# Kernel tuning notes

Measured on AMD Instinct MI355X. Metric: run time of the kernel, lower is better.

The kernel has to match this reference:

```python
import jax, jax.numpy as jnp
import numpy as np

B, N, C, H, K, R = 128, 512, 7, 64, 16, 2
EPS = 1e-5


def setup_inputs() -> dict:
    key = jax.random.key(0)
    ks = jax.random.split(key, 8)
    def w(k, shape, scale):
        return jax.random.normal(k, shape, jnp.float32) * scale
    return {
        'x':    jax.random.normal(ks[0], (B, C, N), jnp.float32),
        # track_mlp: Conv1d(C->H, bias=False) + BN + ReLU, Conv1d(H->H) + BN + ReLU
        'w_t1': w(ks[1], (H, C), 0.3),
        'g_t1': jnp.ones((H,), jnp.float32), 'b_t1': jnp.zeros((H,), jnp.float32),
        'w_t2': w(ks[2], (H, H), 0.15),
        'g_t2': jnp.ones((H,), jnp.float32), 'b_t2': jnp.zeros((H,), jnp.float32),
        # per-round neighbor MLP: Conv1d(2H->H, bias=False) + BN + ReLU (stacked over rounds)
        'w_nb': w(ks[3], (R, H, 2 * H), 0.1),
        'g_nb': jnp.ones((R, H), jnp.float32), 'b_nb': jnp.zeros((R, H), jnp.float32),
        # scorer: Conv1d(H->H, bias=False) + BN + ReLU, Conv1d(H->1, bias=True)
        'w_s1': w(ks[4], (H, H), 0.15),
        'g_s1': jnp.ones((H,), jnp.float32), 'b_s1': jnp.zeros((H,), jnp.float32),
        'w_s2': w(ks[5], (1, H), 0.15), 'b_s2': jnp.zeros((1,), jnp.float32),
    }


def _conv1x1(w, h):
    # Conv1d with kernel_size=1, no bias: (O,C) x (B,C,N) -> (B,O,N)
    return jnp.einsum('oc,bcn->bon', w, h)


def _bn(h, g, b):
    # eval-mode BatchNorm1d with running_mean=0, running_var=1
    s = g / jnp.sqrt(1.0 + EPS)
    return h * s[None, :, None] + b[None, :, None]


def _knn_idx(h, k):
    # h: (B,H,N); squared euclidean distances in feature space, k nearest (incl. self)
    sq = jnp.sum(h * h, axis=1)                       # (B,N)
    inner = jnp.einsum('bhn,bhm->bnm', h, h)          # (B,N,N)
    d = sq[:, :, None] + sq[:, None, :] - 2.0 * inner  # (B,N,N)
    _, idx = jax.lax.top_k(-d, k)                     # (B,N,K)
    return jax.lax.stop_gradient(idx)


def _edgeconv_round(h, w, g, b, k):
    idx = _knn_idx(h, k)                              # (B,N,K)
    # gather neighbor features: (B,H,1,N) indexed along last axis -> (B,H,N,K)
    nbr = jnp.take_along_axis(h[:, :, None, :], idx[:, None, :, :], axis=3)
    hc = h[:, :, :, None]                             # (B,H,N,1)
    edge = jnp.concatenate([jnp.broadcast_to(hc, nbr.shape), nbr - hc], axis=1)  # (B,2H,N,K)
    bsz, twoh, n, kk = edge.shape
    m = _conv1x1(w, edge.reshape(bsz, twoh, n * kk))  # (B,H,N*K)
    m = jax.nn.relu(_bn(m, g, b)).reshape(bsz, -1, n, kk)
    return jnp.max(m, axis=3)                          # (B,H,N) max aggregation


def reference(x, w_t1, g_t1, b_t1, w_t2, g_t2, b_t2, w_nb, g_nb, b_nb,
              w_s1, g_s1, b_s1, w_s2, b_s2):
    # shared per-track MLP
    h = jax.nn.relu(_bn(_conv1x1(w_t1, x), g_t1, b_t1))
    h = jax.nn.relu(_bn(_conv1x1(w_t2, h), g_t2, b_t2))
    # kNN message-passing rounds (EdgeConv with max aggregation)
    for r in range(w_nb.shape[0]):
        h = _edgeconv_round(h, w_nb[r], g_nb[r], b_nb[r], K)
    # scorer head -> per-track logits (B,1,N)
    h = jax.nn.relu(_bn(_conv1x1(w_s1, h), g_s1, b_s1))
    logits = _conv1x1(w_s2, h) + b_s2[None, :, None]
    return logits
```

## Files before the change

kernel.cpp:

```cpp
#include <hip/hip_runtime.h>
#include <math.h>

#define Bn 128
#define Nn 512
#define Cc 7
#define Hh 64
#define Kk 16
#define Rr 2
#define EPSf 1e-5f

typedef __attribute__((ext_vector_type(8))) short bf16x8;
typedef __attribute__((ext_vector_type(4))) float f32x4;

#define PLN ((size_t)4194304)

__device__ __forceinline__ void split3(float a, short &hs, short &ms, short &ls) {
    unsigned u  = __float_as_uint(a);
    unsigned hu = u & 0xFFFF0000u;
    float r1 = a - __uint_as_float(hu);
    unsigned mu = __float_as_uint(r1) & 0xFFFF0000u;
    float r2 = r1 - __uint_as_float(mu);
    unsigned lu = __float_as_uint(r2) & 0xFFFF0000u;
    hs = (short)(hu >> 16); ms = (short)(mu >> 16); ls = (short)(lu >> 16);
}

#define MFMA6(acc, AH, AM, AL, BH, BM, BL) \
    acc = __builtin_amdgcn_mfma_f32_16x16x32_bf16(AL, BH, acc, 0, 0, 0); \
    acc = __builtin_amdgcn_mfma_f32_16x16x32_bf16(AM, BM, acc, 0, 0, 0); \
    acc = __builtin_amdgcn_mfma_f32_16x16x32_bf16(AH, BL, acc, 0, 0, 0); \
    acc = __builtin_amdgcn_mfma_f32_16x16x32_bf16(AM, BH, acc, 0, 0, 0); \
    acc = __builtin_amdgcn_mfma_f32_16x16x32_bf16(AH, BM, acc, 0, 0, 0); \
    acc = __builtin_amdgcn_mfma_f32_16x16x32_bf16(AH, BH, acc, 0, 0, 0);

__global__ void k_prep(const float* __restrict__ w_nb, const float* __restrict__ w_t2,
                       const float* __restrict__ w_s1, short* __restrict__ wS)
{
    int i = blockIdx.x * 256 + threadIdx.x;
    short h_, m_, l_;
    if (i < 8192) {
        int r = i >> 12, oc = i & 4095;
        int o = oc >> 6, c = oc & 63;
        const float* wr = w_nb + (size_t)r * Hh * 2 * Hh + (size_t)o * 2 * Hh;
        float wc = wr[c], wd = wr[Hh + c];
        short* base = wS + (size_t)r * 6 * 4096;
        split3(wd, h_, m_, l_);
        base[0 * 4096 + oc] = h_; base[1 * 4096 + oc] = m_; base[2 * 4096 + oc] = l_;
        split3(wc - wd, h_, m_, l_);
        base[3 * 4096 + oc] = h_; base[4 * 4096 + oc] = m_; base[5 * 4096 + oc] = l_;
    } else {
        int which = (i - 8192) >> 12;
        int oc = i & 4095;
        const float* src = which ? w_s1 : w_t2;
        short* base = wS + (size_t)(12 + which * 3) * 4096;
        split3(src[oc], h_, m_, l_);
        base[0 * 4096 + oc] = h_; base[1 * 4096 + oc] = m_; base[2 * 4096 + oc] = l_;
    }
}

__global__ __launch_bounds__(256) void k_t12(
    const float* __restrict__ x,
    const float* __restrict__ w1, const float* __restrict__ g1, const float* __restrict__ b1,
    const short* __restrict__ wS2, const float* __restrict__ g2, const float* __restrict__ b2,
    short* __restrict__ hS, float* __restrict__ sq)
{
    __shared__ short wLDS[3][64 * 80];
    __shared__ short h1S[3][16 * 80];
    __shared__ float sqP[16][4];

    int t  = threadIdx.x;
    int p0 = blockIdx.x * 16;
    int b  = p0 >> 9, n0 = p0 & 511;

#pragma unroll
    for (int it = 0; it < 6; ++it) {
        int f = it * 256 + t;
        int plane = f >> 9, i8 = f & 511;
        int o = i8 >> 3, c8 = i8 & 7;
        uint4 v = ((const uint4*)(wS2 + (size_t)plane * 4096))[i8];
        *(uint4*)&wLDS[plane][o * 80 + c8 * 8] = v;
    }

    {
        int pt = t & 15, ow = t >> 4;
        const float inv = rsqrtf(1.0f + EPSf);
        float xv[Cc];
#pragma unroll
        for (int c = 0; c < Cc; ++c)
            xv[c] = x[(b * Cc + c) * Nn + n0 + pt];
#pragma unroll
        for (int j = 0; j < 4; ++j) {
            int o = ow + 16 * j;
            float acc = 0.0f;
#pragma unroll
            for (int c = 0; c < Cc; ++c)
                acc = fmaf(w1[o * Cc + c], xv[c], acc);
            acc = fmaf(acc, g1[o] * inv, b1[o]);
            acc = fmaxf(acc, 0.0f);
            short hs_, ms_, ls_;
            split3(acc, hs_, ms_, ls_);
            h1S[0][pt * 80 + o] = hs_;
            h1S[1][pt * 80 + o] = ms_;
            h1S[2][pt * 80 + o] = ls_;
        }
    }
    __syncthreads();

    int wv = t >> 6, lane = t & 63, col = lane & 15, quad = lane >> 4;
    const float inv = rsqrtf(1.0f + EPSf);

    f32x4 acc = (f32x4){0.f, 0.f, 0.f, 0.f};
#pragma unroll
    for (int ks = 0; ks < 2; ++ks) {
        int aoff = ks * 32 + quad * 8;
        bf16x8 AH = *(bf16x8*)&h1S[0][col * 80 + aoff];
        bf16x8 AM = *(bf16x8*)&h1S[1][col * 80 + aoff];
        bf16x8 AL = *(bf16x8*)&h1S[2][col * 80 + aoff];
        int boff = (wv * 16 + col) * 80 + aoff;
        bf16x8 BH = *(bf16x8*)&wLDS[0][boff];
        bf16x8 BM = *(bf16x8*)&wLDS[1][boff];
        bf16x8 BL = *(bf16x8*)&wLDS[2][boff];
        MFMA6(acc, AH, AM, AL, BH, BM, BL)
    }

    int o = wv * 16 + col;
    float sc = g2[o] * inv, bo = b2[o];
    float s4[4];
#pragma unroll
    for (int r = 0; r < 4; ++r) {
        int pt = quad * 4 + r;
        float a2 = fmaf(acc[r], sc, bo);
        a2 = fmaxf(a2, 0.0f);
        short hs_, ms_, ls_;
        split3(a2, hs_, ms_, ls_);
        size_t rowp = (size_t)(p0 + pt) * Hh + o;
        hS[0 * PLN + rowp] = hs_;
        hS[1 * PLN + rowp] = ms_;
        hS[2 * PLN + rowp] = ls_;
        s4[r] = a2 * a2;
    }
#pragma unroll
    for (int sh = 1; sh < 16; sh <<= 1) {
#pragma unroll
        for (int r = 0; r < 4; ++r) s4[r] += __shfl_xor(s4[r], sh, 64);
    }
    if (col == 0) {
#pragma unroll
        for (int r = 0; r < 4; ++r) sqP[quad * 4 + r][wv] = s4[r];
    }
    __syncthreads();
    if (t < 16) sq[p0 + t] = sqP[t][0] + sqP[t][1] + sqP[t][2] + sqP[t][3];
}

__global__ __launch_bounds__(256, 4) void k_knn(
    const short* __restrict__ hS, const float* __restrict__ sq, int* __restrict__ idxout)
{
    int xcd = blockIdx.x & 7;
    int s_  = blockIdx.x >> 3;
    int b   = xcd + ((s_ >> 5) << 3);
    int n0  = (s_ & 31) << 4;
    int t   = threadIdx.x;

    __shared__ unsigned int keysLDS[16 * 512];
    __shared__ float sqS[512];

    if (t < 128) ((float4*)sqS)[t] = ((const float4*)(sq + (size_t)b * Nn))[t];
    __syncthreads();

    int wv = t >> 6, lane = t & 63, col = lane & 15, quad = lane >> 4;
    const size_t rowbase = (size_t)b * Nn * Hh;

    bf16x8 AH[2], AM[2], AL[2];
    {
        const short* crow = hS + rowbase + (size_t)(n0 + col) * Hh;
#pragma unroll
        for (int ks = 0; ks < 2; ++ks) {
            int aoff = ks * 32 + quad * 8;
            AH[ks] = *(const bf16x8*)(crow + 0 * PLN + aoff);
            AM[ks] = *(const bf16x8*)(crow + 1 * PLN + aoff);
            AL[ks] = *(const bf16x8*)(crow + 2 * PLN + aoff);
        }
    }
    float sqcr[4];
#pragma unroll
    for (int r_ = 0; r_ < 4; ++r_) sqcr[r_] = sqS[n0 + quad * 4 + r_];

    for (int i = 0; i < 8; ++i) {
        int nt = wv * 8 + i;
        const short* prow = hS + rowbase + (size_t)(nt * 16 + col) * Hh;
        f32x4 acc = (f32x4){0.f, 0.f, 0.f, 0.f};
#pragma unroll
        for (int ks = 0; ks < 2; ++ks) {
            int aoff = ks * 32 + quad * 8;
            bf16x8 BH = *(const bf16x8*)(prow + 0 * PLN + aoff);
            bf16x8 BM = *(const bf16x8*)(prow + 1 * PLN + aoff);
            bf16x8 BL = *(const bf16x8*)(prow + 2 * PLN + aoff);
            MFMA6(acc, AH[ks], AM[ks], AL[ks], BH, BM, BL)
        }
        float sqp = sqS[nt * 16 + col];
#pragma unroll
        for (int r_ = 0; r_ < 4; ++r_) {
            int ctr = quad * 4 + r_;
            float d = sqcr[r_] + sqp - 2.0f * acc[r_];
            unsigned int u = __float_as_uint(d);
            u = ((int)u < 0) ? ~u : (u | 0x80000000u);
            keysLDS[ctr * 512 + nt * 16 + col] = u;
        }
    }
    __syncthreads();

    for (int pass = 0; pass < 2; ++pass) {
        unsigned int kk[2][8];
        int rr[2][8];
#pragma unroll
        for (int s = 0; s < 2; ++s) {
            int jj = wv * 4 + pass * 2 + s;
            const uint4* kp = (const uint4*)&keysLDS[jj * 512 + (lane << 3)];
            uint4 A = kp[0], Bq = kp[1];
            kk[s][0] = A.x;  kk[s][1] = A.y;  kk[s][2] = A.z;  kk[s][3] = A.w;
            kk[s][4] = Bq.x; kk[s][5] = Bq.y; kk[s][6] = Bq.z; kk[s][7] = Bq.w;
#pragma unroll
            for (int q = 0; q < 8; ++q) rr[s][q] = q;
        }

#define CE(s, i, j_) { \
    bool sw = (kk[s][i] > kk[s][j_]) || (kk[s][i] == kk[s][j_] && rr[s][i] > rr[s][j_]); \
    unsigned int tk = sw ? kk[s][i] : kk[s][j_]; kk[s][i] = sw ? kk[s][j_] : kk[s][i]; kk[s][j_] = tk; \
    int tr = sw ? rr[s][i] : rr[s][j_]; rr[s][i] = sw ? rr[s][j_] : rr[s][i]; rr[s][j_] = tr; }
#pragma unroll
        for (int s = 0; s < 2; ++s) {
            CE(s,0,1) CE(s,2,3) CE(s,4,5) CE(s,6,7)
            CE(s,0,2) CE(s,1,3) CE(s,4,6) CE(s,5,7)
            CE(s,1,2) CE(s,5,6)
            CE(s,0,4) CE(s,1,5) CE(s,2,6) CE(s,3,7)
            CE(s,2,4) CE(s,3,5)
            CE(s,1,2) CE(s,3,4) CE(s,5,6)
        }
#undef CE

        int outbase[2];
#pragma unroll
        for (int s = 0; s < 2; ++s)
            outbase[s] = (b * Nn + n0 + wv * 4 + pass * 2 + s) * Kk;

        for (int iter = 0; iter < Kk; ++iter) {
            unsigned int mv[2];
#pragma unroll
            for (int s = 0; s < 2; ++s) mv[s] = kk[s][0];
#define DSTEP(ctrl) { \
        _Pragma("unroll") \
        for (int s = 0; s < 2; ++s) { \
            unsigned int ov = (unsigned int)__builtin_amdgcn_update_dpp((int)mv[s], (int)mv[s], ctrl, 0xF, 0xF, false); \
            mv[s] = (ov < mv[s]) ? ov : mv[s]; } }
            DSTEP(0xB1)
            DSTEP(0x4E)
            DSTEP(0x124)
            DSTEP(0x128)
            DSTEP(0x142)
            DSTEP(0x143)
#undef DSTEP
            unsigned int m[2];
#pragma unroll
            for (int s = 0; s < 2; ++s)
                m[s] = (unsigned int)__builtin_amdgcn_readlane((int)mv[s], 63);
#pragma unroll
            for (int s = 0; s < 2; ++s) {
                unsigned long long bal = __ballot(kk[s][0] == m[s]);
                int wn = __ffsll(bal) - 1;
                if (lane == wn) {
                    idxout[outbase[s] + iter] = (lane << 3) + rr[s][0];
#pragma unroll
                    for (int q = 0; q < 7; ++q) { kk[s][q] = kk[s][q + 1]; rr[s][q] = rr[s][q + 1]; }
                    kk[s][7] = 0xFFFFFFFFu;
                }
            }
        }
    }
}

__global__ __launch_bounds__(256, 4) void k_edge(
    const short* __restrict__ hS,
    const int* __restrict__ idx,
    const short* __restrict__ wS,
    const float* __restrict__ g, const float* __restrict__ bb_,
    short* __restrict__ hSout, float* __restrict__ sqout)
{
    __shared__ short wLDS[3][64 * 72];
    __shared__ float baseS[16 * 68];
    __shared__ int   idxS[256];

    int t   = threadIdx.x;
    int xcd = blockIdx.x & 7;
    int s_  = blockIdx.x >> 3;
    int b   = xcd + ((s_ >> 5) << 3);
    int p0  = b * Nn + ((s_ & 31) << 4);

    idxS[t] = idx[p0 * Kk + t];
#pragma unroll
    for (int it = 0; it < 6; ++it) {
        int f = it * 256 + t;
        int plane = f >> 9;
        int i8 = f & 511;
        int o = i8 >> 3, c8 = i8 & 7;
        uint4 v = ((const uint4*)(wS + (size_t)(3 + plane) * 4096))[i8];
        *(uint4*)&wLDS[plane][o * 72 + c8 * 8] = v;
    }
    __syncthreads();

    int wv = t >> 6, lane = t & 63, col = lane & 15, quad = lane >> 4;

    {
        f32x4 bacc = (f32x4){0.f, 0.f, 0.f, 0.f};
        const short* hrow = hS + (size_t)(p0 + col) * Hh;
#pragma unroll
        for (int ks = 0; ks < 2; ++ks) {
            int aoff = ks * 32 + quad * 8;
            bf16x8 AH = *(const bf16x8*)(hrow + 0 * PLN + aoff);
            bf16x8 AM = *(const bf16x8*)(hrow + 1 * PLN + aoff);
            bf16x8 AL = *(const bf16x8*)(hrow + 2 * PLN + aoff);
            int boff = (wv * 16 + col) * 72 + aoff;
            bf16x8 BH = *(bf16x8*)&wLDS[0][boff];
            bf16x8 BM = *(bf16x8*)&wLDS[1][boff];
            bf16x8 BL = *(bf16x8*)&wLDS[2][boff];
            MFMA6(bacc, AH, AM, AL, BH, BM, BL)
        }
#pragma unroll
        for (int r_ = 0; r_ < 4; ++r_)
            baseS[(quad * 4 + r_) * 68 + wv * 16 + col] = bacc[r_];
    }
    __syncthreads();

#pragma unroll
    for (int it = 0; it < 6; ++it) {
        int f = it * 256 + t;
        int plane = f >> 9;
        int i8 = f & 511;
        int o = i8 >> 3, c8 = i8 & 7;
        uint4 v = ((const uint4*)(wS + (size_t)plane * 4096))[i8];
        *(uint4*)&wLDS[plane][o * 72 + c8 * 8] = v;
    }
    __syncthreads();

    const float inv = rsqrtf(1.0f + EPSf);
    float scv[4], bov[4];
#pragma unroll
    for (int nt = 0; nt < 4; ++nt) {
        scv[nt] = g[nt * 16 + col] * inv;
        bov[nt] = bb_[nt * 16 + col];
    }

    for (int pr = 0; pr < 2; ++pr) {
        bf16x8 A[2][2][3];
#pragma unroll
        for (int pt2 = 0; pt2 < 2; ++pt2) {
            int pl = wv * 4 + pr * 2 + pt2;
            int j = idxS[pl * 16 + col];
            const short* nrow = hS + ((size_t)(b * Nn) + j) * Hh;
#pragma unroll
            for (int ks = 0; ks < 2; ++ks) {
                int aoff = ks * 32 + quad * 8;
                A[pt2][ks][0] = *(const bf16x8*)(nrow + 0 * PLN + aoff);
                A[pt2][ks][1] = *(const bf16x8*)(nrow + 1 * PLN + aoff);
                A[pt2][ks][2] = *(const bf16x8*)(nrow + 2 * PLN + aoff);
            }
        }

        f32x4 acc[2][4];
#pragma unroll
        for (int pt2 = 0; pt2 < 2; ++pt2)
#pragma unroll
            for (int nt = 0; nt < 4; ++nt)
                acc[pt2][nt] = (f32x4){0.f, 0.f, 0.f, 0.f};

#pragma unroll
        for (int ks = 0; ks < 2; ++ks)
#pragma unroll
            for (int nt = 0; nt < 4; ++nt) {
                int boff = (nt * 16 + col) * 72 + ks * 32 + quad * 8;
                bf16x8 BH = *(bf16x8*)&wLDS[0][boff];
                bf16x8 BM = *(bf16x8*)&wLDS[1][boff];
                bf16x8 BL = *(bf16x8*)&wLDS[2][boff];
#pragma unroll
                for (int pt2 = 0; pt2 < 2; ++pt2) {
                    f32x4 a = acc[pt2][nt];
                    MFMA6(a, A[pt2][ks][0], A[pt2][ks][1], A[pt2][ks][2], BH, BM, BL)
                    acc[pt2][nt] = a;
                }
            }

#pragma unroll
        for (int pt2 = 0; pt2 < 2; ++pt2) {
            int pl = wv * 4 + pr * 2 + pt2;
            int pglob = p0 + pl;
            float res[4];
#pragma unroll
            for (int nt = 0; nt < 4; ++nt) {
                float base = baseS[pl * 68 + nt * 16 + col];
                f32x4 a = acc[pt2][nt];
                float v0 = fmaf(base + a[0], scv[nt], bov[nt]);
                float v1 = fmaf(base + a[1], scv[nt], bov[nt]);
                float v2 = fmaf(base + a[2], scv[nt], bov[nt]);
                float v3 = fmaf(base + a[3], scv[nt], bov[nt]);
                float vm = fmaxf(fmaxf(v0, v1), fmaxf(v2, v3));
                vm = fmaxf(vm, __shfl_xor(vm, 16));
                vm = fmaxf(vm, __shfl_xor(vm, 32));
                res[nt] = fmaxf(vm, 0.0f);
            }
            float rv = res[quad];
            short hs_, ms_, ls_;
            split3(rv, hs_, ms_, ls_);
            hSout[0 * PLN + (size_t)pglob * Hh + lane] = hs_;
            hSout[1 * PLN + (size_t)pglob * Hh + lane] = ms_;
            hSout[2 * PLN + (size_t)pglob * Hh + lane] = ls_;

            float s = res[0] * res[0] + res[1] * res[1]
                    + res[2] * res[2] + res[3] * res[3];
            s += __shfl_xor(s, 1);
            s += __shfl_xor(s, 2);
            s += __shfl_xor(s, 4);
            s += __shfl_xor(s, 8);
            if (lane == 0) sqout[pglob] = s;
        }
    }
}

__global__ __launch_bounds__(256) void k_head(
    const short* __restrict__ hS, const short* __restrict__ wSs1,
    const float* __restrict__ g1, const float* __restrict__ b1,
    const float* __restrict__ w2, const float* __restrict__ b2,
    float* __restrict__ out)
{
    __shared__ short wLDS[3][64 * 80];
    __shared__ float partS[16][4];

    int t  = threadIdx.x;
    int p0 = blockIdx.x * 16;

#pragma unroll
    for (int it = 0; it < 6; ++it) {
        int f = it * 256 + t;
        int plane = f >> 9, i8 = f & 511;
        int o = i8 >> 3, c8 = i8 & 7;
        uint4 v = ((const uint4*)(wSs1 + (size_t)plane * 4096))[i8];
        *(uint4*)&wLDS[plane][o * 80 + c8 * 8] = v;
    }
    __syncthreads();

    int wv = t >> 6, lane = t & 63, col = lane & 15, quad = lane >> 4;

    const short* crow = hS + (size_t)(p0 + col) * Hh;
    f32x4 acc = (f32x4){0.f, 0.f, 0.f, 0.f};
#pragma unroll
    for (int ks = 0; ks < 2; ++ks) {
        int aoff = ks * 32 + quad * 8;
        bf16x8 AH = *(const bf16x8*)(crow + 0 * PLN + aoff);
        bf16x8 AM = *(const bf16x8*)(crow + 1 * PLN + aoff);
        bf16x8 AL = *(const bf16x8*)(crow + 2 * PLN + aoff);
        int boff = (wv * 16 + col) * 80 + aoff;
        bf16x8 BH = *(bf16x8*)&wLDS[0][boff];
        bf16x8 BM = *(bf16x8*)&wLDS[1][boff];
        bf16x8 BL = *(bf16x8*)&wLDS[2][boff];
        MFMA6(acc, AH, AM, AL, BH, BM, BL)
    }

    int o = wv * 16 + col;
    const float inv = rsqrtf(1.0f + EPSf);
    float sc = g1[o] * inv, bo = b1[o], w2o = w2[o];
    float s4[4];
#pragma unroll
    for (int r = 0; r < 4; ++r) {
        float a = fmaxf(fmaf(acc[r], sc, bo), 0.0f);
        s4[r] = a * w2o;
    }
#pragma unroll
    for (int sh = 1; sh < 16; sh <<= 1) {
#pragma unroll
        for (int r = 0; r < 4; ++r) s4[r] += __shfl_xor(s4[r], sh, 64);
    }
    if (col == 0) {
#pragma unroll
        for (int r = 0; r < 4; ++r) partS[quad * 4 + r][wv] = s4[r];
    }
    __syncthreads();
    if (t < 16)
        out[p0 + t] = partS[t][0] + partS[t][1] + partS[t][2] + partS[t][3] + b2[0];
}

extern "C" void kernel_launch(void* const* d_in, const int* in_sizes, int n_in,
                              void* d_out, int out_size, void* d_ws, size_t ws_size,
                              hipStream_t stream)
{
    const float* x    = (const float*)d_in[0];
    const float* w_t1 = (const float*)d_in[1];
    const float* g_t1 = (const float*)d_in[2];
    const float* b_t1 = (const float*)d_in[3];
    const float* w_t2 = (const float*)d_in[4];
    const float* g_t2 = (const float*)d_in[5];
    const float* b_t2 = (const float*)d_in[6];
    const float* w_nb = (const float*)d_in[7];
    const float* g_nb = (const float*)d_in[8];
    const float* b_nb = (const float*)d_in[9];
    const float* w_s1 = (const float*)d_in[10];
    const float* g_s1 = (const float*)d_in[11];
    const float* b_s1 = (const float*)d_in[12];
    const float* w_s2 = (const float*)d_in[13];
    const float* b_s2 = (const float*)d_in[14];
    float* out = (float*)d_out;

    float* sq  = (float*)d_ws;
    int*   idx = (int*)(sq + (size_t)Bn * Nn);
    short* hSa = (short*)(idx + (size_t)Bn * Nn * Kk);
    short* hSb = hSa + 3 * PLN;
    short* wS  = hSb + 3 * PLN;

    k_prep<<<64, 256, 0, stream>>>(w_nb, w_t2, w_s1, wS);
    k_t12<<<Bn * Nn / 16, 256, 0, stream>>>(x, w_t1, g_t1, b_t1,
                                            wS + (size_t)12 * 4096, g_t2, b_t2,
                                            hSa, sq);

    const short* hSin = hSa;
    short* hSout = hSb;
    for (int r = 0; r < Rr; ++r) {
        k_knn<<<Bn * (Nn / 16), 256, 0, stream>>>(hSin, sq, idx);
        k_edge<<<Bn * Nn / 16, 256, 0, stream>>>(hSin, idx,
            wS + (size_t)r * 6 * 4096, g_nb + r * Hh, b_nb + r * Hh,
            hSout, sq);
        const short* ts = hSout; hSout = (short*)hSin; hSin = ts;
    }
    k_head<<<Bn * Nn / 16, 256, 0, stream>>>(hSin, wS + (size_t)15 * 4096,
                                             g_s1, b_s1, w_s2, b_s2, out);
}
```

Measured before the change: 473.7 us.

## Fuse kNN selection and EdgeConv into one kernel with shared LDS union

Merges the kNN top-k kernel and the EdgeConv kernel into a single launch per round. Neighbour indices now stay in shared memory instead of being written to and re-read from global memory. The key buffer and the weight/base buffers share one LDS union so shared-memory use does not grow. The squared-norm buffer is now double-buffered, because the fused kernel reads the old norms while writing new ones. This removes one launch per round and the idx round trip through global memory, at the cost of a longer kernel with more barriers and possibly different occupancy.

```diff
diff --git a/kernel.cpp b/kernel.cpp
--- a/kernel.cpp
+++ b/kernel.cpp
@@ -151,26 +151,39 @@
     if (t < 16) sq[p0 + t] = sqP[t][0] + sqP[t][1] + sqP[t][2] + sqP[t][3];
 }
 
-__global__ __launch_bounds__(256, 4) void k_knn(
-    const short* __restrict__ hS, const float* __restrict__ sq, int* __restrict__ idxout)
+union KnnEdgeLDS {
+    unsigned int keys[16 * 512];
+    struct {
+        short wLDS[3][64 * 72];
+        float baseS[16 * 68];
+    } p2;
+};
+
+__global__ __launch_bounds__(256, 4) void k_knn_edge(
+    const short* __restrict__ hS, const float* __restrict__ sqin,
+    const short* __restrict__ wS,
+    const float* __restrict__ g, const float* __restrict__ bb_,
+    short* __restrict__ hSout, float* __restrict__ sqout)
 {
+    __shared__ KnnEdgeLDS u;
+    __shared__ float sqS[512];
+    __shared__ int   idxS[256];
+
+    int t   = threadIdx.x;
     int xcd = blockIdx.x & 7;
     int s_  = blockIdx.x >> 3;
     int b   = xcd + ((s_ >> 5) << 3);
     int n0  = (s_ & 31) << 4;
-    int t   = threadIdx.x;
-
-    __shared__ unsigned int keysLDS[16 * 512];
-    __shared__ float sqS[512];
-
-    if (t < 128) ((float4*)sqS)[t] = ((const float4*)(sq + (size_t)b * Nn))[t];
+    int p0  = b * Nn + n0;
+
+    if (t < 128) ((float4*)sqS)[t] = ((const float4*)(sqin + (size_t)b * Nn))[t];
     __syncthreads();
 
     int wv = t >> 6, lane = t & 63, col = lane & 15, quad = lane >> 4;
     const size_t rowbase = (size_t)b * Nn * Hh;
 
-    bf16x8 AH[2], AM[2], AL[2];
     {
+        bf16x8 AH[2], AM[2], AL[2];
         const short* crow = hS + rowbase + (size_t)(n0 + col) * Hh;
 #pragma unroll
         for (int ks = 0; ks < 2; ++ks) {
@@ -179,31 +192,31 @@
             AM[ks] = *(const bf16x8*)(crow + 1 * PLN + aoff);
             AL[ks] = *(const bf16x8*)(crow + 2 * PLN + aoff);
         }
-    }
-    float sqcr[4];
-#pragma unroll
-    for (int r_ = 0; r_ < 4; ++r_) sqcr[r_] = sqS[n0 + quad * 4 + r_];
-
-    for (int i = 0; i < 8; ++i) {
-        int nt = wv * 8 + i;
-        const short* prow = hS + rowbase + (size_t)(nt * 16 + col) * Hh;
-        f32x4 acc = (f32x4){0.f, 0.f, 0.f, 0.f};
-#pragma unroll
-        for (int ks = 0; ks < 2; ++ks) {
-            int aoff = ks * 32 + quad * 8;
-            bf16x8 BH = *(const bf16x8*)(prow + 0 * PLN + aoff);
-            bf16x8 BM = *(const bf16x8*)(prow + 1 * PLN + aoff);
-            bf16x8 BL = *(const bf16x8*)(prow + 2 * PLN + aoff);
-            MFMA6(acc, AH[ks], AM[ks], AL[ks], BH, BM, BL)
-        }
-        float sqp = sqS[nt * 16 + col];
-#pragma unroll
-        for (int r_ = 0; r_ < 4; ++r_) {
-            int ctr = quad * 4 + r_;
-            float d = sqcr[r_] + sqp - 2.0f * acc[r_];
-            unsigned int u = __float_as_uint(d);
-            u = ((int)u < 0) ? ~u : (u | 0x80000000u);
-            keysLDS[ctr * 512 + nt * 16 + col] = u;
+        float sqcr[4];
+#pragma unroll
+        for (int r_ = 0; r_ < 4; ++r_) sqcr[r_] = sqS[n0 + quad * 4 + r_];
+
+        for (int i = 0; i < 8; ++i) {
+            int nt = wv * 8 + i;
+            const short* prow = hS + rowbase + (size_t)(nt * 16 + col) * Hh;
+            f32x4 acc = (f32x4){0.f, 0.f, 0.f, 0.f};
+#pragma unroll
+            for (int ks = 0; ks < 2; ++ks) {
+                int aoff = ks * 32 + quad * 8;
+                bf16x8 BH = *(const bf16x8*)(prow + 0 * PLN + aoff);
+                bf16x8 BM = *(const bf16x8*)(prow + 1 * PLN + aoff);
+                bf16x8 BL = *(const bf16x8*)(prow + 2 * PLN + aoff);
+                MFMA6(acc, AH[ks], AM[ks], AL[ks], BH, BM, BL)
+            }
+            float sqp = sqS[nt * 16 + col];
+#pragma unroll
+            for (int r_ = 0; r_ < 4; ++r_) {
+                int ctr = quad * 4 + r_;
+                float d = sqcr[r_] + sqp - 2.0f * acc[r_];
+                unsigned int uu = __float_as_uint(d);
+                uu = ((int)uu < 0) ? ~uu : (uu | 0x80000000u);
+                u.keys[ctr * 512 + nt * 16 + col] = uu;
+            }
         }
     }
     __syncthreads();
@@ -214,7 +227,7 @@
 #pragma unroll
         for (int s = 0; s < 2; ++s) {
             int jj = wv * 4 + pass * 2 + s;
-            const uint4* kp = (const uint4*)&keysLDS[jj * 512 + (lane << 3)];
+            const uint4* kp = (const uint4*)&u.keys[jj * 512 + (lane << 3)];
             uint4 A = kp[0], Bq = kp[1];
             kk[s][0] = A.x;  kk[s][1] = A.y;  kk[s][2] = A.z;  kk[s][3] = A.w;
             kk[s][4] = Bq.x; kk[s][5] = Bq.y; kk[s][6] = Bq.z; kk[s][7] = Bq.w;
@@ -240,7 +253,7 @@
         int outbase[2];
 #pragma unroll
         for (int s = 0; s < 2; ++s)
-            outbase[s] = (b * Nn + n0 + wv * 4 + pass * 2 + s) * Kk;
+            outbase[s] = (wv * 4 + pass * 2 + s) * Kk;
 
         for (int iter = 0; iter < Kk; ++iter) {
             unsigned int mv[2];
@@ -267,7 +280,7 @@
                 unsigned long long bal = __ballot(kk[s][0] == m[s]);
                 int wn = __ffsll(bal) - 1;
                 if (lane == wn) {
-                    idxout[outbase[s] + iter] = (lane << 3) + rr[s][0];
+                    idxS[outbase[s] + iter] = (lane << 3) + rr[s][0];
 #pragma unroll
                     for (int q = 0; q < 7; ++q) { kk[s][q] = kk[s][q + 1]; rr[s][q] = rr[s][q + 1]; }
                     kk[s][7] = 0xFFFFFFFFu;
@@ -275,26 +288,8 @@
             }
         }
     }
-}
-
-__global__ __launch_bounds__(256, 4) void k_edge(
-    const short* __restrict__ hS,
-    const int* __restrict__ idx,
-    const short* __restrict__ wS,
-    const float* __restrict__ g, const float* __restrict__ bb_,
-    short* __restrict__ hSout, float* __restrict__ sqout)
-{
-    __shared__ short wLDS[3][64 * 72];
-    __shared__ float baseS[16 * 68];
-    __shared__ int   idxS[256];
-
-    int t   = threadIdx.x;
-    int xcd = blockIdx.x & 7;
-    int s_  = blockIdx.x >> 3;
-    int b   = xcd + ((s_ >> 5) << 3);
-    int p0  = b * Nn + ((s_ & 31) << 4);
-
-    idxS[t] = idx[p0 * Kk + t];
+    __syncthreads();
+
 #pragma unroll
     for (int it = 0; it < 6; ++it) {
         int f = it * 256 + t;
@@ -302,11 +297,9 @@
         int i8 = f & 511;
         int o = i8 >> 3, c8 = i8 & 7;
         uint4 v = ((const uint4*)(wS + (size_t)(3 + plane) * 4096))[i8];
-        *(uint4*)&wLDS[plane][o * 72 + c8 * 8] = v;
-    }
-    __syncthreads();
-
-    int wv = t >> 6, lane = t & 63, col = lane & 15, quad = lane >> 4;
+        *(uint4*)&u.p2.wLDS[plane][o * 72 + c8 * 8] = v;
+    }
+    __syncthreads();
 
     {
         f32x4 bacc = (f32x4){0.f, 0.f, 0.f, 0.f};
@@ -318,14 +311,14 @@
             bf16x8 AM = *(const bf16x8*)(hrow + 1 * PLN + aoff);
             bf16x8 AL = *(const bf16x8*)(hrow + 2 * PLN + aoff);
             int boff = (wv * 16 + col) * 72 + aoff;
-            bf16x8 BH = *(bf16x8*)&wLDS[0][boff];
-            bf16x8 BM = *(bf16x8*)&wLDS[1][boff];
-            bf16x8 BL = *(bf16x8*)&wLDS[2][boff];
+            bf16x8 BH = *(bf16x8*)&u.p2.wLDS[0][boff];
+            bf16x8 BM = *(bf16x8*)&u.p2.wLDS[1][boff];
+            bf16x8 BL = *(bf16x8*)&u.p2.wLDS[2][boff];
             MFMA6(bacc, AH, AM, AL, BH, BM, BL)
         }
 #pragma unroll
         for (int r_ = 0; r_ < 4; ++r_)
-            baseS[(quad * 4 + r_) * 68 + wv * 16 + col] = bacc[r_];
+            u.p2.baseS[(quad * 4 + r_) * 68 + wv * 16 + col] = bacc[r_];
     }
     __syncthreads();
 
@@ -336,7 +329,7 @@
         int i8 = f & 511;
         int o = i8 >> 3, c8 = i8 & 7;
         uint4 v = ((const uint4*)(wS + (size_t)plane * 4096))[i8];
-        *(uint4*)&wLDS[plane][o * 72 + c8 * 8] = v;
+        *(uint4*)&u.p2.wLDS[plane][o * 72 + c8 * 8] = v;
     }
     __syncthreads();
 
@@ -376,9 +369,9 @@
 #pragma unroll
             for (int nt = 0; nt < 4; ++nt) {
                 int boff = (nt * 16 + col) * 72 + ks * 32 + quad * 8;
-                bf16x8 BH = *(bf16x8*)&wLDS[0][boff];
-                bf16x8 BM = *(bf16x8*)&wLDS[1][boff];
-                bf16x8 BL = *(bf16x8*)&wLDS[2][boff];
+                bf16x8 BH = *(bf16x8*)&u.p2.wLDS[0][boff];
+                bf16x8 BM = *(bf16x8*)&u.p2.wLDS[1][boff];
+                bf16x8 BL = *(bf16x8*)&u.p2.wLDS[2][boff];
 #pragma unroll
                 for (int pt2 = 0; pt2 < 2; ++pt2) {
                     f32x4 a = acc[pt2][nt];
@@ -394,7 +387,7 @@
             float res[4];
 #pragma unroll
             for (int nt = 0; nt < 4; ++nt) {
-                float base = baseS[pl * 68 + nt * 16 + col];
+                float base = u.p2.baseS[pl * 68 + nt * 16 + col];
                 f32x4 a = acc[pt2][nt];
                 float v0 = fmaf(base + a[0], scv[nt], bov[nt]);
                 float v1 = fmaf(base + a[1], scv[nt], bov[nt]);
@@ -506,25 +499,25 @@
     const float* b_s2 = (const float*)d_in[14];
     float* out = (float*)d_out;
 
-    float* sq  = (float*)d_ws;
-    int*   idx = (int*)(sq + (size_t)Bn * Nn);
-    short* hSa = (short*)(idx + (size_t)Bn * Nn * Kk);
+    float* sqA = (float*)d_ws;
+    float* sqB = sqA + (size_t)Bn * Nn;
+    short* hSa = (short*)(sqB + (size_t)Bn * Nn);
     short* hSb = hSa + 3 * PLN;
     short* wS  = hSb + 3 * PLN;
 
     k_prep<<<64, 256, 0, stream>>>(w_nb, w_t2, w_s1, wS);
     k_t12<<<Bn * Nn / 16, 256, 0, stream>>>(x, w_t1, g_t1, b_t1,
                                             wS + (size_t)12 * 4096, g_t2, b_t2,
-                                            hSa, sq);
-
-    const short* hSin = hSa;
-    short* hSout = hSb;
+                                            hSa, sqA);
+
+    const short* hSin = hSa;  short* hSout = hSb;
+    const float* sqin = sqA;  float* sqo   = sqB;
     for (int r = 0; r < Rr; ++r) {
-        k_knn<<<Bn * (Nn / 16), 256, 0, stream>>>(hSin, sq, idx);
-        k_edge<<<Bn * Nn / 16, 256, 0, stream>>>(hSin, idx,
+        k_knn_edge<<<Bn * (Nn / 16), 256, 0, stream>>>(hSin, sqin,
             wS + (size_t)r * 6 * 4096, g_nb + r * Hh, b_nb + r * Hh,
-            hSout, sq);
+            hSout, sqo);
         const short* ts = hSout; hSout = (short*)hSin; hSin = ts;
+        const float* tq = sqo;   sqo   = (float*)sqin; sqin = tq;
     }
     k_head<<<Bn * Nn / 16, 256, 0, stream>>>(hSin, wS + (size_t)15 * 4096,
                                              g_s1, b_s1, w_s2, b_s2, out);
```

After: 466.2 us. No clear change (-1.6%).
